# Kernel tuning notes

Measured on AMD Instinct MI355X. Metric: run time of the kernel, lower is better.

Reference implementation:

```python
import jax, jax.numpy as jnp
import numpy as np

N_NODES = 50000
N_REL = 3
N_EDGES = 500000
D_IN, D_HID, D_OUT = 128, 256, 128


def setup_inputs() -> dict:
    key = jax.random.key(0)
    ks = jax.random.split(key, 9)
    def w(k, shape, fan_in):
        return jax.random.normal(k, shape, dtype=jnp.float32) / np.sqrt(fan_in)
    return {
        "x": jax.random.normal(ks[0], (N_NODES, D_IN), dtype=jnp.float32),
        "src": jax.random.randint(ks[1], (N_REL, N_EDGES), 0, N_NODES, dtype=jnp.int32),
        "dst": jax.random.randint(ks[2], (N_REL, N_EDGES), 0, N_NODES, dtype=jnp.int32),
        "w_self1": w(ks[3], (N_REL, D_IN, D_HID), D_IN),
        "w_neigh1": w(ks[4], (N_REL, D_IN, D_HID), D_IN),
        "b1": jnp.zeros((N_REL, D_HID), dtype=jnp.float32),
        "w_self2": w(ks[5], (N_REL, D_HID, D_OUT), D_HID),
        "w_neigh2": w(ks[6], (N_REL, D_HID, D_OUT), D_HID),
        "b2": jnp.zeros((N_REL, D_OUT), dtype=jnp.float32),
    }


def _sage_hetero_layer(x, src, dst, w_self, w_neigh, b):
    """Multi-relation SAGEConv (mean agg); relation outputs summed (HeteroGraphConv default).
    x: [N, din]; src/dst: [R, E]; w_*: [R, din, dout]; b: [R, dout]."""
    n = x.shape[0]

    def per_rel(s, d, ws, wn, bb):
        gathered = jnp.take(x, s, axis=0)                      # [E, din] neighbor gather
        summed = jax.ops.segment_sum(gathered, d, num_segments=n)  # [N, din]
        deg = jax.ops.segment_sum(jnp.ones(s.shape, jnp.float32), d, num_segments=n)
        h_neigh = summed / jnp.maximum(deg, 1.0)[:, None]      # mean, 0 for isolated dst
        return x @ ws + h_neigh @ wn + bb                      # fc_self + fc_neigh + bias

    per_rel_out = jax.vmap(per_rel)(src, dst, w_self, w_neigh, b)  # [R, N, dout]
    return per_rel_out.sum(axis=0)


def reference(x, src, dst, w_self1, w_neigh1, b1, w_self2, w_neigh2, b2):
    h = _sage_hetero_layer(x, src, dst, w_self1, w_neigh1, b1)
    h = jax.nn.relu(h)  # SAGEConv activation in hidden layers
    out = _sage_hetero_layer(h, src, dst, w_self2, w_neigh2, b2)  # last layer: no activation
    return out
```

## Files before the change

kernel.cpp:

```cpp
#include <hip/hip_runtime.h>

#define NN 50000
#define NREL 3
#define NE 500000
#define DIN 128
#define DHID 256
#define DOUT 128

#define NBUK 98
#define CAP 8192
#define EPB 2048
#define NCHK ((NE + EPB - 1) / EPB)
#define PA_BLKS (NREL * NCHK)
#define F2B_BLKS 6250
#define ZROW ((uint)NN << 8)

typedef unsigned int uint;
typedef unsigned short ushort;
typedef __attribute__((ext_vector_type(8))) short bf16x8;
typedef __attribute__((ext_vector_type(4))) float f32x4;
typedef __attribute__((ext_vector_type(2))) float f32x2;

using gptr_t = const __attribute__((address_space(1))) unsigned int*;
using lptr_t = __attribute__((address_space(3))) unsigned int*;

__device__ __forceinline__ ushort f2bf(float f) {
    uint u = __float_as_uint(f);
    uint r = (u + 0x7fffu + ((u >> 16) & 1u)) >> 16;
    return (ushort)r;
}
__device__ __forceinline__ void acc2(f32x2& a, uint u) {
    f32x2 t;
    t.x = __uint_as_float(u << 16);
    t.y = __uint_as_float(u & 0xffff0000u);
    a += t;
}
__device__ __forceinline__ void acc16(f32x2* a, uint4 v) {
    acc2(a[0], v.x); acc2(a[1], v.y); acc2(a[2], v.z); acc2(a[3], v.w);
}

__global__ __launch_bounds__(256) void pass_a_prep(
    const int* __restrict__ src, const int* __restrict__ dst,
    int* __restrict__ bcursor, uint* __restrict__ pairs,
    const float* __restrict__ x, ushort* __restrict__ xb,
    const float* __restrict__ ws1, const float* __restrict__ wn1, ushort* __restrict__ Bt1,
    const float* __restrict__ ws2, const float* __restrict__ wn2, ushort* __restrict__ Bt2,
    const float* __restrict__ b1, float* __restrict__ bsum1,
    const float* __restrict__ b2, float* __restrict__ bsum2,
    ushort* __restrict__ agg0, ushort* __restrict__ agg1, ushort* __restrict__ agg2) {
    int blk = blockIdx.x, tid = threadIdx.x;
    if (blk < PA_BLKS) {
        int r = blk / NCHK;
        int chunk = blk % NCHK;
        int e0 = chunk * EPB;
        int nedge = min(EPB, NE - e0);
        const int* S = src + (size_t)r * NE + e0;
        const int* D = dst + (size_t)r * NE + e0;
        __shared__ int cnt[NBUK], base[NBUK], cur[NBUK];
        if (tid < NBUK) { cnt[tid] = 0; cur[tid] = 0; }
        __syncthreads();
        uint pk[8];
        int bk[8];
        bool val[8];
#pragma unroll
        for (int j = 0; j < 8; ++j) {
            int e = j * 256 + tid;
            val[j] = e < nedge;
            int d = val[j] ? D[e] : 0;
            int s = val[j] ? S[e] : 0;
            bk[j] = d >> 9;
            pk[j] = ((uint)s << 9) | (uint)(d & 511);
            if (val[j]) atomicAdd(&cnt[bk[j]], 1);
        }
        __syncthreads();
        if (tid < NBUK) base[tid] = atomicAdd(&bcursor[r * NBUK + tid], cnt[tid]);
        __syncthreads();
#pragma unroll
        for (int j = 0; j < 8; ++j) {
            if (val[j]) {
                int slot = base[bk[j]] + atomicAdd(&cur[bk[j]], 1);
                if (slot < CAP) pairs[(size_t)(r * NBUK + bk[j]) * CAP + slot] = pk[j];
            }
        }
        return;
    }
    blk -= PA_BLKS;
    if (blk < F2B_BLKS) {
        int t = blk * 256 + tid;
        float4 v = *(const float4*)(x + (size_t)t * 4);
        uint2 p;
        p.x = (uint)f2bf(v.x) | ((uint)f2bf(v.y) << 16);
        p.y = (uint)f2bf(v.z) | ((uint)f2bf(v.w) << 16);
        *(uint2*)(xb + (size_t)t * 4) = p;
    } else if (blk < F2B_BLKS + 512) {
        int t = (blk - F2B_BLKS) * 256 + tid;
        int n = t >> 9, k = t & 511;
        int b = k >> 7, kk = k & 127;
        float v;
        if (b == 0)
            v = ws1[kk * 256 + n] + ws1[128 * 256 + kk * 256 + n] + ws1[2 * 128 * 256 + kk * 256 + n];
        else
            v = wn1[(size_t)(b - 1) * 128 * 256 + kk * 256 + n];
        Bt1[t] = f2bf(v);
    } else if (blk < F2B_BLKS + 1024) {
        int t = (blk - F2B_BLKS - 512) * 256 + tid;
        int n = t >> 8, k = t & 255;
        int c = n >> 7, j = n & 127;
        float v;
        if (c == 0)
            v = ws2[k * 128 + j] + ws2[256 * 128 + k * 128 + j] + ws2[2 * 256 * 128 + k * 128 + j];
        else
            v = wn2[(size_t)(c - 1) * 256 * 128 + k * 128 + j];
        Bt2[t] = f2bf(v);
    } else {
        if (tid < DHID) bsum1[tid] = b1[tid] + b1[DHID + tid] + b1[2 * DHID + tid];
        if (tid < DOUT) bsum2[tid] = b2[tid] + b2[DOUT + tid] + b2[2 * DOUT + tid];
        if (tid >= 192 && tid < 256) {
            int b = (tid - 192) >> 4, i = tid & 15;
            ushort* row = (b == 0) ? xb : (b == 1) ? agg0 : (b == 2) ? agg1 : agg2;
            uint4 z = {0u, 0u, 0u, 0u};
            *(uint4*)(row + (size_t)NN * 128 + i * 8) = z;
        }
    }
}

__global__ __launch_bounds__(256) void pass_b(const uint* __restrict__ pairs,
                                              const int* __restrict__ bcnt,
                                              uint* __restrict__ srclist,
                                              int2* __restrict__ nd) {
    int blk = blockIdx.x;
    int b = blk % NBUK;
    int r = blk / NBUK;
    int node_base = b * 512;
    int count = min(bcnt[blk], CAP);
    int obase = blk * CAP;
    const uint* pp = pairs + (size_t)blk * CAP;
    __shared__ int hist[512];
    __shared__ int cur[512];
    __shared__ int sc[256];
    int tid = threadIdx.x;
    hist[tid] = 0;
    hist[tid + 256] = 0;
    __syncthreads();
    for (int i = tid; i < count; i += 256) atomicAdd(&hist[pp[i] & 511], 1);
    __syncthreads();
    int v0 = hist[2 * tid], v1 = hist[2 * tid + 1];
    int p0 = (v0 + 7) & ~7;
    int p1 = (v1 + 7) & ~7;
    int s = p0 + p1;
    sc[tid] = s;
    __syncthreads();
    for (int st = 1; st < 256; st <<= 1) {
        int t = (tid >= st) ? sc[tid - st] : 0;
        __syncthreads();
        sc[tid] += t;
        __syncthreads();
    }
    int excl = sc[tid] - s;
    int c0 = obase + excl;
    int c1 = c0 + p0;
    cur[2 * tid] = c0;
    cur[2 * tid + 1] = c1;
    int n0 = node_base + 2 * tid;
    if (n0 < NN)     nd[r * NN + n0]     = make_int2(v0, c0);
    if (n0 + 1 < NN) nd[r * NN + n0 + 1] = make_int2(v1, c1);
    __syncthreads();
    for (int i = tid; i < count; i += 256) {
        uint p = pp[i];
        int pos = atomicAdd(&cur[p & 511], 1);
        srclist[pos] = (p >> 1) & ~255u;
    }
    __syncthreads();
    for (int i = v0; i < p0; ++i) srclist[c0 + i] = ZROW;
    for (int i = v1; i < p1; ++i) srclist[c1 + i] = ZROW;
}

template <int PHASE>
__global__ __launch_bounds__(256) void gather3(
    const ushort* __restrict__ f0, const ushort* __restrict__ f1,
    const ushort* __restrict__ f2, const int2* __restrict__ nd,
    const uint* __restrict__ srclist,
    ushort* __restrict__ ob, float* __restrict__ of) {
    int node = blockIdx.x * 4 + (threadIdx.x >> 6);
    if (node >= NN) return;
    int lane = threadIdx.x & 63;
    int g = lane >> 4;
    uint c16 = (uint)(lane & 15) * 16;
    const char* fp0 = (const char*)f0;
    const char* fp1 = (const char*)f1;
    const char* fp2 = (const char*)f2;

    int2 q0 = nd[node];
    int2 q1 = nd[NN + node];
    int2 q2 = nd[2 * NN + node];
    int d0 = q0.x, d1 = q1.x, d2 = q2.x;
    int pd0 = (d0 + 7) & ~7, pd1 = (d1 + 7) & ~7, pd2 = (d2 + 7) & ~7;
    uint sid0 = srclist[q0.y + lane];
    uint sid1 = srclist[q1.y + lane];
    uint sid2 = srclist[q2.y + lane];

    f32x2 a0[4], a1[4], a2[4];
#pragma unroll
    for (int k = 0; k < 4; ++k) { a0[k] = 0.f; a1[k] = 0.f; a2[k] = 0.f; }

    uint zoff = ZROW + c16;
    int pmax = max(max(pd0, pd1), pd2);
    int pm64 = min(pmax, 64);
    for (int j0 = 0; j0 < pm64; j0 += 8) {
        uint oA = (j0 < pd0) ? (__shfl(sid0, j0 + g) + c16) : zoff;
        uint oB = (j0 < pd0) ? (__shfl(sid0, j0 + 4 + g) + c16) : zoff;
        uint oC = (j0 < pd1) ? (__shfl(sid1, j0 + g) + c16) : zoff;
        uint oD = (j0 < pd1) ? (__shfl(sid1, j0 + 4 + g) + c16) : zoff;
        uint oE = (j0 < pd2) ? (__shfl(sid2, j0 + g) + c16) : zoff;
        uint oF = (j0 < pd2) ? (__shfl(sid2, j0 + 4 + g) + c16) : zoff;
        uint4 vA = *(const uint4*)(fp0 + oA);
        uint4 vB = *(const uint4*)(fp0 + oB);
        uint4 vC = *(const uint4*)(fp1 + oC);
        uint4 vD = *(const uint4*)(fp1 + oD);
        uint4 vE = *(const uint4*)(fp2 + oE);
        uint4 vF = *(const uint4*)(fp2 + oF);
        acc16(a0, vA); acc16(a0, vB);
        acc16(a1, vC); acc16(a1, vD);
        acc16(a2, vE); acc16(a2, vF);
    }
    if (pmax > 64) {
        for (int i0 = 64; i0 < pd0; i0 += 64) {
            uint sl = srclist[q0.y + i0 + lane];
            int lim = min(pd0 - i0, 64);
            for (int j0 = 0; j0 < lim; j0 += 8) {
                uint u1 = __shfl(sl, j0 + g) + c16, u2 = __shfl(sl, j0 + 4 + g) + c16;
                acc16(a0, *(const uint4*)(fp0 + u1));
                acc16(a0, *(const uint4*)(fp0 + u2));
            }
        }
        for (int i0 = 64; i0 < pd1; i0 += 64) {
            uint sl = srclist[q1.y + i0 + lane];
            int lim = min(pd1 - i0, 64);
            for (int j0 = 0; j0 < lim; j0 += 8) {
                uint u1 = __shfl(sl, j0 + g) + c16, u2 = __shfl(sl, j0 + 4 + g) + c16;
                acc16(a1, *(const uint4*)(fp1 + u1));
                acc16(a1, *(const uint4*)(fp1 + u2));
            }
        }
        for (int i0 = 64; i0 < pd2; i0 += 64) {
            uint sl = srclist[q2.y + i0 + lane];
            int lim = min(pd2 - i0, 64);
            for (int j0 = 0; j0 < lim; j0 += 8) {
                uint u1 = __shfl(sl, j0 + g) + c16, u2 = __shfl(sl, j0 + 4 + g) + c16;
                acc16(a2, *(const uint4*)(fp2 + u1));
                acc16(a2, *(const uint4*)(fp2 + u2));
            }
        }
    }

#pragma unroll
    for (int k = 0; k < 4; ++k) {
        a0[k].x += __shfl_xor(a0[k].x, 16); a0[k].y += __shfl_xor(a0[k].y, 16);
        a0[k].x += __shfl_xor(a0[k].x, 32); a0[k].y += __shfl_xor(a0[k].y, 32);
        a1[k].x += __shfl_xor(a1[k].x, 16); a1[k].y += __shfl_xor(a1[k].y, 16);
        a1[k].x += __shfl_xor(a1[k].x, 32); a1[k].y += __shfl_xor(a1[k].y, 32);
        a2[k].x += __shfl_xor(a2[k].x, 16); a2[k].y += __shfl_xor(a2[k].y, 16);
        a2[k].x += __shfl_xor(a2[k].x, 32); a2[k].y += __shfl_xor(a2[k].y, 32);
    }
    float inv0 = 1.f / fmaxf((float)d0, 1.f);
    float inv1 = 1.f / fmaxf((float)d1, 1.f);
    float inv2 = 1.f / fmaxf((float)d2, 1.f);
    if (PHASE == 0) {
        if (g == 0) {
            size_t base = (size_t)node * 128 + (c16 >> 1);
            size_t rstride = (size_t)(NN + 1) * DIN;
            uint4 pk;
            pk.x = (uint)f2bf(a0[0].x * inv0) | ((uint)f2bf(a0[0].y * inv0) << 16);
            pk.y = (uint)f2bf(a0[1].x * inv0) | ((uint)f2bf(a0[1].y * inv0) << 16);
            pk.z = (uint)f2bf(a0[2].x * inv0) | ((uint)f2bf(a0[2].y * inv0) << 16);
            pk.w = (uint)f2bf(a0[3].x * inv0) | ((uint)f2bf(a0[3].y * inv0) << 16);
            *(uint4*)(ob + base) = pk;
            pk.x = (uint)f2bf(a1[0].x * inv1) | ((uint)f2bf(a1[0].y * inv1) << 16);
            pk.y = (uint)f2bf(a1[1].x * inv1) | ((uint)f2bf(a1[1].y * inv1) << 16);
            pk.z = (uint)f2bf(a1[2].x * inv1) | ((uint)f2bf(a1[2].y * inv1) << 16);
            pk.w = (uint)f2bf(a1[3].x * inv1) | ((uint)f2bf(a1[3].y * inv1) << 16);
            *(uint4*)(ob + rstride + base) = pk;
            pk.x = (uint)f2bf(a2[0].x * inv2) | ((uint)f2bf(a2[0].y * inv2) << 16);
            pk.y = (uint)f2bf(a2[1].x * inv2) | ((uint)f2bf(a2[1].y * inv2) << 16);
            pk.z = (uint)f2bf(a2[2].x * inv2) | ((uint)f2bf(a2[2].y * inv2) << 16);
            pk.w = (uint)f2bf(a2[3].x * inv2) | ((uint)f2bf(a2[3].y * inv2) << 16);
            *(uint4*)(ob + 2 * rstride + base) = pk;
        }
    } else {
        if (g == 0) {
            float* po = of + (size_t)node * 128 + (c16 >> 1);
            float4 a = *(float4*)po;
            float4 b = *(float4*)(po + 4);
            a.x += a0[0].x * inv0 + a1[0].x * inv1 + a2[0].x * inv2;
            a.y += a0[0].y * inv0 + a1[0].y * inv1 + a2[0].y * inv2;
            a.z += a0[1].x * inv0 + a1[1].x * inv1 + a2[1].x * inv2;
            a.w += a0[1].y * inv0 + a1[1].y * inv1 + a2[1].y * inv2;
            b.x += a0[2].x * inv0 + a1[2].x * inv1 + a2[2].x * inv2;
            b.y += a0[2].y * inv0 + a1[2].y * inv1 + a2[2].y * inv2;
            b.z += a0[3].x * inv0 + a1[3].x * inv1 + a2[3].x * inv2;
            b.w += a0[3].y * inv0 + a1[3].y * inv1 + a2[3].y * inv2;
            *(float4*)po = a;
            *(float4*)(po + 4) = b;
        }
    }
}

template <int LAYER>
__global__ __launch_bounds__(512) void gemm_mfma(
    const ushort* __restrict__ A0, const ushort* __restrict__ A1,
    const ushort* __restrict__ A2, const ushort* __restrict__ A3,
    const ushort* __restrict__ Bt, const float* __restrict__ bias,
    ushort* __restrict__ HO, float* __restrict__ CO,
    ushort* __restrict__ Y1, ushort* __restrict__ Y2, ushort* __restrict__ Y3) {
    constexpr int KTOT = (LAYER == 1) ? 512 : 256;
    constexpr int ASTRIDE = (LAYER == 1) ? 128 : 256;
    __shared__ __align__(16) ushort As[128 * 32];
    __shared__ __align__(16) ushort Bs[256 * 32];

    const int tid = threadIdx.x, lane = tid & 63, w = tid >> 6;
    const int wr = w >> 2, wc = w & 3;
    const int bm = blockIdx.x * 128;
    const int bn = blockIdx.y * 256;

    f32x4 acc[4][4];
#pragma unroll
    for (int m = 0; m < 4; ++m)
#pragma unroll
        for (int n = 0; n < 4; ++n) acc[m][n] = (f32x4){0.f, 0.f, 0.f, 0.f};

    const int srow = tid >> 2;
    const int schunk = (tid & 3) * 8;

    for (int k0 = 0; k0 < KTOT; k0 += 32) {
        const ushort* Ab = A0;
        int koff = k0;
        if (LAYER == 1) {
            int b = k0 >> 7;
            Ab = (b == 0) ? A0 : (b == 1) ? A1 : (b == 2) ? A2 : A3;
            koff = k0 & 127;
        }
        {
            const ushort* srcA = Ab + (size_t)(bm + srow) * ASTRIDE + koff + schunk;
            __builtin_amdgcn_global_load_lds((gptr_t)srcA, (lptr_t)(As + w * 512), 16, 0, 0);
        }
#pragma unroll
        for (int i = 0; i < 2; ++i) {
            int row = i * 128 + srow;
            const ushort* srcB = Bt + (size_t)(bn + row) * KTOT + k0 + schunk;
            __builtin_amdgcn_global_load_lds((gptr_t)srcB, (lptr_t)(Bs + i * 4096 + w * 512), 16, 0, 0);
        }
        __syncthreads();

        const int r = lane & 15, g = lane >> 4;
        bf16x8 af[4], bg[4];
#pragma unroll
        for (int m = 0; m < 4; ++m)
            af[m] = *(const bf16x8*)&As[(wr * 64 + m * 16 + r) * 32 + g * 8];
#pragma unroll
        for (int n = 0; n < 4; ++n)
            bg[n] = *(const bf16x8*)&Bs[(wc * 64 + n * 16 + r) * 32 + g * 8];
#pragma unroll
        for (int m = 0; m < 4; ++m)
#pragma unroll
            for (int n = 0; n < 4; ++n)
                acc[m][n] = __builtin_amdgcn_mfma_f32_16x16x32_bf16(af[m], bg[n], acc[m][n], 0, 0, 0);
        __syncthreads();
    }

    const int r = lane & 15, g = lane >> 4;
    if (LAYER == 1) {
#pragma unroll
        for (int m = 0; m < 4; ++m)
#pragma unroll
            for (int v = 0; v < 4; ++v) {
                int gm = bm + wr * 64 + m * 16 + g * 4 + v;
                if (gm >= NN) continue;
#pragma unroll
                for (int n = 0; n < 4; ++n) {
                    int gn = wc * 64 + n * 16 + r;
                    float f = acc[m][n][v] + bias[gn];
                    f = fmaxf(f, 0.f);
                    HO[(size_t)gm * 256 + gn] = f2bf(f);
                }
            }
    } else {
        int buf = (bn >> 7) + (wc >> 1);
        ushort* Y = (buf == 1) ? Y1 : (buf == 2) ? Y2 : Y3;
#pragma unroll
        for (int m = 0; m < 4; ++m)
#pragma unroll
            for (int v = 0; v < 4; ++v) {
                int gm = bm + wr * 64 + m * 16 + g * 4 + v;
                if (gm >= NN) continue;
#pragma unroll
                for (int n = 0; n < 4; ++n) {
                    int col = (wc & 1) * 64 + n * 16 + r;
                    if (buf == 0)
                        CO[(size_t)gm * 128 + col] = acc[m][n][v] + bias[col];
                    else
                        Y[(size_t)gm * 128 + col] = f2bf(acc[m][n][v]);
                }
            }
    }
}

extern "C" void kernel_launch(void* const* d_in, const int* in_sizes, int n_in,
                              void* d_out, int out_size, void* d_ws, size_t ws_size,
                              hipStream_t stream) {
    const float* x        = (const float*)d_in[0];
    const int*   src      = (const int*)d_in[1];
    const int*   dst      = (const int*)d_in[2];
    const float* w_self1  = (const float*)d_in[3];
    const float* w_neigh1 = (const float*)d_in[4];
    const float* b1       = (const float*)d_in[5];
    const float* w_self2  = (const float*)d_in[6];
    const float* w_neigh2 = (const float*)d_in[7];
    const float* b2       = (const float*)d_in[8];
    float* out = (float*)d_out;

    char* ws = (char*)d_ws;
    size_t off = 0;
    auto alloc = [&](size_t bytes) {
        char* p = ws + off;
        off += (bytes + 255) & ~(size_t)255;
        return p;
    };
    const size_t NROW = NN + 1;
    int*    bcursor = (int*)alloc(NREL * NBUK * 4);
    int2*   nd      = (int2*)alloc((size_t)NREL * NN * 8);
    uint*   srclist = (uint*)alloc(((size_t)NREL * NBUK * CAP + 256) * 4);
    float*  bsum1   = (float*)alloc(DHID * 4);
    float*  bsum2   = (float*)alloc(DOUT * 4);
    ushort* Bt1     = (ushort*)alloc((size_t)DHID * 512 * 2);
    ushort* Bt2     = (ushort*)alloc((size_t)512 * DHID * 2);
    ushort* xb      = (ushort*)alloc(NROW * DIN * 2);
    ushort* aggb    = (ushort*)alloc((size_t)NREL * NROW * DIN * 2);
    ushort* Hb      = (ushort*)alloc((size_t)NN * DHID * 2);
    (void)alloc(65536);
    uint* pairs = (uint*)Hb;
    ushort* agg0 = aggb;
    ushort* agg1 = aggb + NROW * DIN;
    ushort* agg2 = aggb + 2 * NROW * DIN;

    hipMemsetAsync(bcursor, 0, NREL * NBUK * 4, stream);
    pass_a_prep<<<PA_BLKS + F2B_BLKS + 1024 + 1, 256, 0, stream>>>(
        src, dst, bcursor, pairs,
        x, xb, w_self1, w_neigh1, Bt1, w_self2, w_neigh2, Bt2,
        b1, bsum1, b2, bsum2, agg0, agg1, agg2);
    pass_b<<<NREL * NBUK, 256, 0, stream>>>(pairs, bcursor, srclist, nd);

    int ggrid = (NN + 3) / 4;

    gather3<0><<<ggrid, 256, 0, stream>>>(xb, xb, xb, nd, srclist, aggb, nullptr);
    {
        dim3 grid((NN + 127) / 128, 1);
        gemm_mfma<1><<<grid, 512, 0, stream>>>(
            xb, agg0, agg1, agg2, Bt1, bsum1, Hb, nullptr, nullptr, nullptr, nullptr);
    }
    {
        dim3 grid((NN + 127) / 128, 2);
        gemm_mfma<2><<<grid, 512, 0, stream>>>(
            Hb, nullptr, nullptr, nullptr, Bt2, bsum2,
            nullptr, out, agg0, agg1, agg2);
    }
    gather3<1><<<ggrid, 256, 0, stream>>>(
        agg0, agg1, agg2, nd, srclist, nullptr, out);
}
```

Baseline: 239.8 us.

## Overlap layer-1 self GEMM with neighbor gather in a single fused launch

The layer-1 x@W_self product (K=128) moves into the gather launch as extra MFMA blocks. These run next to the memory-bound neighbor-gather blocks and write a bf16 partial into Hb. The remaining layer-1 GEMM then covers only the three aggregated blocks (K=384) and adds the stored self partial before bias and ReLU. The bucketing pass also doubles edges per block. The cost is an extra bf16 round trip through Hb and an additional rounding of the self partial.

```diff
diff --git a/kernel.cpp b/kernel.cpp
--- a/kernel.cpp
+++ b/kernel.cpp
@@ -9,11 +9,12 @@
 
 #define NBUK 98
 #define CAP 8192
-#define EPB 2048
+#define EPB 4096
 #define NCHK ((NE + EPB - 1) / EPB)
 #define PA_BLKS (NREL * NCHK)
 #define F2B_BLKS 6250
 #define ZROW ((uint)NN << 8)
+#define MM1S_BLKS 782
 
 typedef unsigned int uint;
 typedef unsigned short ushort;
@@ -59,11 +60,11 @@
         __shared__ int cnt[NBUK], base[NBUK], cur[NBUK];
         if (tid < NBUK) { cnt[tid] = 0; cur[tid] = 0; }
         __syncthreads();
-        uint pk[8];
-        int bk[8];
-        bool val[8];
-#pragma unroll
-        for (int j = 0; j < 8; ++j) {
+        uint pk[16];
+        int bk[16];
+        bool val[16];
+#pragma unroll
+        for (int j = 0; j < 16; ++j) {
             int e = j * 256 + tid;
             val[j] = e < nedge;
             int d = val[j] ? D[e] : 0;
@@ -76,7 +77,7 @@
         if (tid < NBUK) base[tid] = atomicAdd(&bcursor[r * NBUK + tid], cnt[tid]);
         __syncthreads();
 #pragma unroll
-        for (int j = 0; j < 8; ++j) {
+        for (int j = 0; j < 16; ++j) {
             if (val[j]) {
                 int slot = base[bk[j]] + atomicAdd(&cur[bk[j]], 1);
                 if (slot < CAP) pairs[(size_t)(r * NBUK + bk[j]) * CAP + slot] = pk[j];
@@ -176,14 +177,13 @@
 }
 
 template <int PHASE>
-__global__ __launch_bounds__(256) void gather3(
+__device__ __forceinline__ void gather_body(
+    int node, int tid,
     const ushort* __restrict__ f0, const ushort* __restrict__ f1,
     const ushort* __restrict__ f2, const int2* __restrict__ nd,
     const uint* __restrict__ srclist,
     ushort* __restrict__ ob, float* __restrict__ of) {
-    int node = blockIdx.x * 4 + (threadIdx.x >> 6);
-    if (node >= NN) return;
-    int lane = threadIdx.x & 63;
+    int lane = tid & 63;
     int g = lane >> 4;
     uint c16 = (uint)(lane & 15) * 16;
     const char* fp0 = (const char*)f0;
@@ -305,15 +305,92 @@
     }
 }
 
+__global__ __launch_bounds__(256) void g1_fused(
+    const ushort* __restrict__ xb, const int2* __restrict__ nd,
+    const uint* __restrict__ srclist, ushort* __restrict__ aggb,
+    const ushort* __restrict__ Bt1, ushort* __restrict__ Hb) {
+    if (blockIdx.x >= MM1S_BLKS) {
+        int node = (blockIdx.x - MM1S_BLKS) * 4 + (threadIdx.x >> 6);
+        if (node < NN)
+            gather_body<0>(node, threadIdx.x, xb, xb, xb, nd, srclist, aggb, nullptr);
+        return;
+    }
+    __shared__ __align__(16) ushort As[128 * 32];
+    __shared__ __align__(16) ushort Bs[128 * 32];
+    const int tid = threadIdx.x, lane = tid & 63, w = tid >> 6;
+    const int wr = w >> 1, wc = w & 1;
+    const int bm = (blockIdx.x % 391) * 128;
+    const int bn = (blockIdx.x / 391) * 128;
+
+    f32x4 acc[4][4];
+#pragma unroll
+    for (int m = 0; m < 4; ++m)
+#pragma unroll
+        for (int n = 0; n < 4; ++n) acc[m][n] = (f32x4){0.f, 0.f, 0.f, 0.f};
+
+    const int arow = lane >> 2;
+    const int akq = (lane & 3) * 8;
+
+    for (int k0 = 0; k0 < 128; k0 += 32) {
+#pragma unroll
+        for (int i = 0; i < 2; ++i) {
+            int c = w + i * 4;
+            const ushort* srcA = xb + (size_t)(bm + c * 16 + arow) * 128 + k0 + akq;
+            __builtin_amdgcn_global_load_lds((gptr_t)srcA, (lptr_t)(As + c * 512), 16, 0, 0);
+            const ushort* srcB = Bt1 + (size_t)(bn + c * 16 + arow) * 512 + k0 + akq;
+            __builtin_amdgcn_global_load_lds((gptr_t)srcB, (lptr_t)(Bs + c * 512), 16, 0, 0);
+        }
+        __syncthreads();
+        const int r = lane & 15, g = lane >> 4;
+        bf16x8 af[4], bg[4];
+#pragma unroll
+        for (int m = 0; m < 4; ++m)
+            af[m] = *(const bf16x8*)&As[(wr * 64 + m * 16 + r) * 32 + g * 8];
+#pragma unroll
+        for (int n = 0; n < 4; ++n)
+            bg[n] = *(const bf16x8*)&Bs[(wc * 64 + n * 16 + r) * 32 + g * 8];
+#pragma unroll
+        for (int m = 0; m < 4; ++m)
+#pragma unroll
+            for (int n = 0; n < 4; ++n)
+                acc[m][n] = __builtin_amdgcn_mfma_f32_16x16x32_bf16(af[m], bg[n], acc[m][n], 0, 0, 0);
+        __syncthreads();
+    }
+    const int r = lane & 15, g = lane >> 4;
+#pragma unroll
+    for (int m = 0; m < 4; ++m)
+#pragma unroll
+        for (int v = 0; v < 4; ++v) {
+            int gm = bm + wr * 64 + m * 16 + g * 4 + v;
+            if (gm >= NN) continue;
+#pragma unroll
+            for (int n = 0; n < 4; ++n) {
+                int gn = bn + wc * 64 + n * 16 + r;
+                Hb[(size_t)gm * 256 + gn] = f2bf(acc[m][n][v]);
+            }
+        }
+}
+
+__global__ __launch_bounds__(256) void gather_p1(
+    const ushort* __restrict__ f0, const ushort* __restrict__ f1,
+    const ushort* __restrict__ f2, const int2* __restrict__ nd,
+    const uint* __restrict__ srclist, float* __restrict__ of) {
+    int node = blockIdx.x * 4 + (threadIdx.x >> 6);
+    if (node < NN)
+        gather_body<1>(node, threadIdx.x, f0, f1, f2, nd, srclist, nullptr, of);
+}
+
 template <int LAYER>
 __global__ __launch_bounds__(512) void gemm_mfma(
     const ushort* __restrict__ A0, const ushort* __restrict__ A1,
-    const ushort* __restrict__ A2, const ushort* __restrict__ A3,
-    const ushort* __restrict__ Bt, const float* __restrict__ bias,
+    const ushort* __restrict__ A2, const ushort* __restrict__ Bt,
+    const float* __restrict__ bias,
     ushort* __restrict__ HO, float* __restrict__ CO,
     ushort* __restrict__ Y1, ushort* __restrict__ Y2, ushort* __restrict__ Y3) {
-    constexpr int KTOT = (LAYER == 1) ? 512 : 256;
+    constexpr int KTOT = (LAYER == 1) ? 384 : 256;
     constexpr int ASTRIDE = (LAYER == 1) ? 128 : 256;
+    constexpr int BSTRIDE = (LAYER == 1) ? 512 : 256;
+    constexpr int BKOFF = (LAYER == 1) ? 128 : 0;
     __shared__ __align__(16) ushort As[128 * 32];
     __shared__ __align__(16) ushort Bs[256 * 32];
 
@@ -336,7 +413,7 @@
         int koff = k0;
         if (LAYER == 1) {
             int b = k0 >> 7;
-            Ab = (b == 0) ? A0 : (b == 1) ? A1 : (b == 2) ? A2 : A3;
+            Ab = (b == 0) ? A0 : (b == 1) ? A1 : A2;
             koff = k0 & 127;
         }
         {
@@ -346,7 +423,7 @@
 #pragma unroll
         for (int i = 0; i < 2; ++i) {
             int row = i * 128 + srow;
-            const ushort* srcB = Bt + (size_t)(bn + row) * KTOT + k0 + schunk;
+            const ushort* srcB = Bt + (size_t)(bn + row) * BSTRIDE + BKOFF + k0 + schunk;
             __builtin_amdgcn_global_load_lds((gptr_t)srcB, (lptr_t)(Bs + i * 4096 + w * 512), 16, 0, 0);
         }
         __syncthreads();
@@ -378,9 +455,10 @@
 #pragma unroll
                 for (int n = 0; n < 4; ++n) {
                     int gn = wc * 64 + n * 16 + r;
-                    float f = acc[m][n][v] + bias[gn];
-                    f = fmaxf(f, 0.f);
-                    HO[(size_t)gm * 256 + gn] = f2bf(f);
+                    size_t idx = (size_t)gm * 256 + gn;
+                    float hself = __uint_as_float(((uint)HO[idx]) << 16);
+                    float f = acc[m][n][v] + hself + bias[gn];
+                    HO[idx] = f2bf(fmaxf(f, 0.f));
                 }
             }
     } else {
@@ -451,18 +529,17 @@
 
     int ggrid = (NN + 3) / 4;
 
-    gather3<0><<<ggrid, 256, 0, stream>>>(xb, xb, xb, nd, srclist, aggb, nullptr);
+    g1_fused<<<MM1S_BLKS + ggrid, 256, 0, stream>>>(xb, nd, srclist, aggb, Bt1, Hb);
     {
         dim3 grid((NN + 127) / 128, 1);
         gemm_mfma<1><<<grid, 512, 0, stream>>>(
-            xb, agg0, agg1, agg2, Bt1, bsum1, Hb, nullptr, nullptr, nullptr, nullptr);
+            agg0, agg1, agg2, Bt1, bsum1, Hb, nullptr, nullptr, nullptr, nullptr);
     }
     {
         dim3 grid((NN + 127) / 128, 2);
         gemm_mfma<2><<<grid, 512, 0, stream>>>(
-            Hb, nullptr, nullptr, nullptr, Bt2, bsum2,
+            Hb, nullptr, nullptr, Bt2, bsum2,
             nullptr, out, agg0, agg1, agg2);
     }
-    gather3<1><<<ggrid, 256, 0, stream>>>(
-        agg0, agg1, agg2, nd, srclist, nullptr, out);
-}
+    gather_p1<<<ggrid, 256, 0, stream>>>(agg0, agg1, agg2, nd, srclist, out);
+}
```

After: 272.5 us. +13.7%, slower.

## Double-buffer GEMM LDS tiles and enlarge edge bucketing chunks

Applied to the files above, without the earlier changes.

The MFMA GEMM now uses two LDS buffers per operand and prefetches the next K tile with global_load_lds while computing on the current one. Explicit vmcnt waits and raw s_barrier calls replace __syncthreads. Edge bucketing now processes 4096 edges per block instead of 2048, halving those blocks and their global cursor atomics. The gather kernel becomes a device body wrapped by two thin kernels. Risks are higher LDS use lowering occupancy and correctness depending on the hand-written vmcnt count.

```diff
diff --git a/kernel.cpp b/kernel.cpp
--- a/kernel.cpp
+++ b/kernel.cpp
@@ -9,7 +9,7 @@
 
 #define NBUK 98
 #define CAP 8192
-#define EPB 2048
+#define EPB 4096
 #define NCHK ((NE + EPB - 1) / EPB)
 #define PA_BLKS (NREL * NCHK)
 #define F2B_BLKS 6250
@@ -59,11 +59,11 @@
         __shared__ int cnt[NBUK], base[NBUK], cur[NBUK];
         if (tid < NBUK) { cnt[tid] = 0; cur[tid] = 0; }
         __syncthreads();
-        uint pk[8];
-        int bk[8];
-        bool val[8];
-#pragma unroll
-        for (int j = 0; j < 8; ++j) {
+        uint pk[16];
+        int bk[16];
+        bool val[16];
+#pragma unroll
+        for (int j = 0; j < 16; ++j) {
             int e = j * 256 + tid;
             val[j] = e < nedge;
             int d = val[j] ? D[e] : 0;
@@ -76,7 +76,7 @@
         if (tid < NBUK) base[tid] = atomicAdd(&bcursor[r * NBUK + tid], cnt[tid]);
         __syncthreads();
 #pragma unroll
-        for (int j = 0; j < 8; ++j) {
+        for (int j = 0; j < 16; ++j) {
             if (val[j]) {
                 int slot = base[bk[j]] + atomicAdd(&cur[bk[j]], 1);
                 if (slot < CAP) pairs[(size_t)(r * NBUK + bk[j]) * CAP + slot] = pk[j];
@@ -176,14 +176,13 @@
 }
 
 template <int PHASE>
-__global__ __launch_bounds__(256) void gather3(
+__device__ __forceinline__ void gather_body(
+    int node, int tid,
     const ushort* __restrict__ f0, const ushort* __restrict__ f1,
     const ushort* __restrict__ f2, const int2* __restrict__ nd,
     const uint* __restrict__ srclist,
     ushort* __restrict__ ob, float* __restrict__ of) {
-    int node = blockIdx.x * 4 + (threadIdx.x >> 6);
-    if (node >= NN) return;
-    int lane = threadIdx.x & 63;
+    int lane = tid & 63;
     int g = lane >> 4;
     uint c16 = (uint)(lane & 15) * 16;
     const char* fp0 = (const char*)f0;
@@ -305,6 +304,23 @@
     }
 }
 
+__global__ __launch_bounds__(256) void gather_p0(
+    const ushort* __restrict__ xb, const int2* __restrict__ nd,
+    const uint* __restrict__ srclist, ushort* __restrict__ aggb) {
+    int node = blockIdx.x * 4 + (threadIdx.x >> 6);
+    if (node < NN)
+        gather_body<0>(node, threadIdx.x, xb, xb, xb, nd, srclist, aggb, nullptr);
+}
+
+__global__ __launch_bounds__(256) void gather_p1(
+    const ushort* __restrict__ f0, const ushort* __restrict__ f1,
+    const ushort* __restrict__ f2, const int2* __restrict__ nd,
+    const uint* __restrict__ srclist, float* __restrict__ of) {
+    int node = blockIdx.x * 4 + (threadIdx.x >> 6);
+    if (node < NN)
+        gather_body<1>(node, threadIdx.x, f0, f1, f2, nd, srclist, nullptr, of);
+}
+
 template <int LAYER>
 __global__ __launch_bounds__(512) void gemm_mfma(
     const ushort* __restrict__ A0, const ushort* __restrict__ A1,
@@ -314,24 +330,25 @@
     ushort* __restrict__ Y1, ushort* __restrict__ Y2, ushort* __restrict__ Y3) {
     constexpr int KTOT = (LAYER == 1) ? 512 : 256;
     constexpr int ASTRIDE = (LAYER == 1) ? 128 : 256;
-    __shared__ __align__(16) ushort As[128 * 32];
-    __shared__ __align__(16) ushort Bs[256 * 32];
+    constexpr int NT = KTOT / 32;
+    __shared__ __align__(16) ushort As[2][128 * 32];
+    __shared__ __align__(16) ushort Bs[2][256 * 32];
 
     const int tid = threadIdx.x, lane = tid & 63, w = tid >> 6;
     const int wr = w >> 2, wc = w & 3;
     const int bm = blockIdx.x * 128;
     const int bn = blockIdx.y * 256;
-
-    f32x4 acc[4][4];
-#pragma unroll
-    for (int m = 0; m < 4; ++m)
-#pragma unroll
-        for (int n = 0; n < 4; ++n) acc[m][n] = (f32x4){0.f, 0.f, 0.f, 0.f};
-
     const int srow = tid >> 2;
     const int schunk = (tid & 3) * 8;
 
-    for (int k0 = 0; k0 < KTOT; k0 += 32) {
+    f32x4 acc[4][4];
+#pragma unroll
+    for (int m = 0; m < 4; ++m)
+#pragma unroll
+        for (int n = 0; n < 4; ++n) acc[m][n] = (f32x4){0.f, 0.f, 0.f, 0.f};
+
+    auto stage = [&](int t, int buf) {
+        int k0 = t * 32;
         const ushort* Ab = A0;
         int koff = k0;
         if (LAYER == 1) {
@@ -339,35 +356,43 @@
             Ab = (b == 0) ? A0 : (b == 1) ? A1 : (b == 2) ? A2 : A3;
             koff = k0 & 127;
         }
-        {
-            const ushort* srcA = Ab + (size_t)(bm + srow) * ASTRIDE + koff + schunk;
-            __builtin_amdgcn_global_load_lds((gptr_t)srcA, (lptr_t)(As + w * 512), 16, 0, 0);
-        }
+        const ushort* srcA = Ab + (size_t)(bm + srow) * ASTRIDE + koff + schunk;
+        __builtin_amdgcn_global_load_lds((gptr_t)srcA, (lptr_t)(&As[buf][w * 512]), 16, 0, 0);
 #pragma unroll
         for (int i = 0; i < 2; ++i) {
-            int row = i * 128 + srow;
-            const ushort* srcB = Bt + (size_t)(bn + row) * KTOT + k0 + schunk;
-            __builtin_amdgcn_global_load_lds((gptr_t)srcB, (lptr_t)(Bs + i * 4096 + w * 512), 16, 0, 0);
-        }
-        __syncthreads();
-
-        const int r = lane & 15, g = lane >> 4;
+            const ushort* srcB = Bt + (size_t)(bn + i * 128 + srow) * KTOT + k0 + schunk;
+            __builtin_amdgcn_global_load_lds((gptr_t)srcB, (lptr_t)(&Bs[buf][i * 4096 + w * 512]), 16, 0, 0);
+        }
+    };
+
+    stage(0, 0);
+    const int r = lane & 15, g = lane >> 4;
+    for (int t = 0; t < NT; ++t) {
+        int cur = t & 1;
+        if (t + 1 < NT) {
+            stage(t + 1, cur ^ 1);
+            asm volatile("s_waitcnt vmcnt(3)" ::: "memory");
+        } else {
+            asm volatile("s_waitcnt vmcnt(0)" ::: "memory");
+        }
+        __builtin_amdgcn_s_barrier();
+        asm volatile("" ::: "memory");
         bf16x8 af[4], bg[4];
 #pragma unroll
         for (int m = 0; m < 4; ++m)
-            af[m] = *(const bf16x8*)&As[(wr * 64 + m * 16 + r) * 32 + g * 8];
+            af[m] = *(const bf16x8*)&As[cur][(wr * 64 + m * 16 + r) * 32 + g * 8];
 #pragma unroll
         for (int n = 0; n < 4; ++n)
-            bg[n] = *(const bf16x8*)&Bs[(wc * 64 + n * 16 + r) * 32 + g * 8];
+            bg[n] = *(const bf16x8*)&Bs[cur][(wc * 64 + n * 16 + r) * 32 + g * 8];
 #pragma unroll
         for (int m = 0; m < 4; ++m)
 #pragma unroll
             for (int n = 0; n < 4; ++n)
                 acc[m][n] = __builtin_amdgcn_mfma_f32_16x16x32_bf16(af[m], bg[n], acc[m][n], 0, 0, 0);
-        __syncthreads();
-    }
-
-    const int r = lane & 15, g = lane >> 4;
+        asm volatile("" ::: "memory");
+        __builtin_amdgcn_s_barrier();
+    }
+
     if (LAYER == 1) {
 #pragma unroll
         for (int m = 0; m < 4; ++m)
@@ -451,7 +476,7 @@
 
     int ggrid = (NN + 3) / 4;
 
-    gather3<0><<<ggrid, 256, 0, stream>>>(xb, xb, xb, nd, srclist, aggb, nullptr);
+    gather_p0<<<ggrid, 256, 0, stream>>>(xb, nd, srclist, aggb);
     {
         dim3 grid((NN + 127) / 128, 1);
         gemm_mfma<1><<<grid, 512, 0, stream>>>(
@@ -463,6 +488,5 @@
             Hb, nullptr, nullptr, nullptr, Bt2, bsum2,
             nullptr, out, agg0, agg1, agg2);
     }
-    gather3<1><<<ggrid, 256, 0, stream>>>(
-        agg0, agg1, agg2, nd, srclist, nullptr, out);
-}
+    gather_p1<<<ggrid, 256, 0, stream>>>(agg0, agg1, agg2, nd, srclist, out);
+}
```

New measurement: 224.8 us. 6.2% less time.
